# Kernel tuning notes

Hardware: AMD Instinct MI355X
Metric: run time of the kernel (lower is better)

Reference implementation:

```python
import jax, jax.numpy as jnp
import numpy as np

PS = 2      # patch_size
TOPK = 3    # topk


def setup_inputs() -> dict:
    key = jax.random.key(0)
    x = jax.random.normal(key, (16, 128, 64, 64), dtype=jnp.float32)
    alpha = jnp.asarray(5.0, dtype=jnp.float32)
    return {"x": x, "alpha": alpha}


def reference(x, alpha):
    ps = PS
    b, c, h, w = x.shape
    nph, npw = h // ps, w // ps
    npatch = nph * npw
    pa = ps * ps
    # F.normalize(x, p=2, dim=-3): L2-normalize over channels
    nrm = jnp.sqrt(jnp.sum(x * x, axis=1, keepdims=True))
    x = x / jnp.maximum(nrm, 1e-12)
    # patchify: [b,c,h,w] -> [b,c,num_patches,patch_area]
    x = x.reshape(b * c * nph, ps, npw, ps)
    x = jnp.swapaxes(x, 1, 2).reshape(b, c, npatch, pa)
    diag = np.arange(ps) * (ps + 1)          # diagonal positions within a patch
    x = x[:, :, :, diag]                     # [b,c,npatch,ps]
    x = jnp.swapaxes(x, 1, 3)                # [b,ps,npatch,c]
    # per-diagonal-pixel patch correlation matrix
    corr = jnp.einsum('bpnc,bpmc->bpnm', x, x)           # [b,ps,np,np]
    avg = jnp.mean(corr, axis=1, keepdims=True)
    corr = jnp.concatenate([corr, avg], axis=1)          # [b,ps+1,np,np]
    # gaussian self-suppression mask (1 - gaussian centered at each patch)
    rat_s = 0.05
    sr, sc = nph * rat_s, npw * rat_s
    ind_r = jnp.arange(nph, dtype=jnp.float32).reshape(1, nph, 1)
    ind_c = jnp.arange(npw, dtype=jnp.float32).reshape(1, 1, npw)
    cr, cc = jnp.meshgrid(jnp.arange(nph, dtype=jnp.float32),
                          jnp.arange(npw, dtype=jnp.float32), indexing='ij')
    cent_r = cr.reshape(npatch, 1, 1)
    cent_c = cc.reshape(npatch, 1, 1)
    g = jnp.exp(-(ind_r - cent_r) ** 2 / (2.0 * sr * sr)) \
        * jnp.exp(-(ind_c - cent_c) ** 2 / (2.0 * sc * sc))   # [np,nph,npw]
    mask = (1.0 - g).reshape(1, 1, npatch, npatch)
    s = (corr * mask) * alpha
    # dual (row + column) softmax
    a = jax.nn.softmax(s, axis=-1) * jax.nn.softmax(s, axis=-2)  # [b,ps+1,np,np]
    # scatter: diagonal in-patch pixels get their own map, rest get the avg map
    src = np.full(pa, ps, dtype=np.int64)
    src[diag] = np.arange(ps)
    a = a[:, src]                              # [b,pa,np,np]
    # un-patchify attention back to [b, npatch, h, w]
    a = jnp.swapaxes(a, 1, 3)                  # [b,np,np,pa]
    a = a.reshape(b * npatch * nph, npw, ps, ps)
    a = jnp.swapaxes(a, 1, 2)
    a = a.reshape(b, npatch, h, w)
    # top-k over the patch (correlation-source) dim
    vals = jax.lax.top_k(jnp.moveaxis(a, 1, -1), TOPK)[0]  # [b,h,w,k]
    return jnp.moveaxis(vals, -1, 1)           # [b,k,h,w]
```

## Files before the change

kernel.cpp:

```cpp
#include <hip/hip_runtime.h>
#include <math.h>

#define NB 16
#define NCH 128
#define NH 64
#define NW 64
#define NP 1024

#define TN 32
#define TM 128
#define KC 32
#define KP 36
#define PK 40

#define NTILE 144

typedef __attribute__((ext_vector_type(8))) short short8v;
typedef __attribute__((ext_vector_type(4))) float f32x4;

__device__ __forceinline__ float med3(float a, float b, float c) {
  return __builtin_amdgcn_fmed3f(a, b, c);
}
__device__ __forceinline__ void top3_ins(float& t0, float& t1, float& t2, float a) {
  float n0 = fmaxf(t0, a);
  float n1 = med3(a, t0, t1);
  float n2 = med3(a, t1, t2);
  t0 = n0; t1 = n1; t2 = n2;
}
__device__ __forceinline__ float dot4(float4 a, float4 b) {
  return a.x * b.x + a.y * b.y + a.z * b.z + a.w * b.w;
}
__device__ __forceinline__ ushort f2bf(float f) {
  unsigned u = __float_as_uint(f);
  unsigned r = (u + 0x7FFFu + ((u >> 16) & 1u)) >> 16;
  return (ushort)r;
}
__device__ __forceinline__ float bf2f(ushort h) {
  return __uint_as_float(((unsigned)h) << 16);
}

__global__ __launch_bounds__(256) void prep_split(const float* __restrict__ x,
                                                  ushort* __restrict__ Vs,
                                                  float* __restrict__ rsum) {
  int blk = blockIdx.x;
  int t = threadIdx.x;
  int gid = blk * 256 + t;
  if (gid < NB * 3 * NP) rsum[gid] = 0.f;

  int b = blk >> 5;
  int c = (blk >> 4) & 1;
  int ng = blk & 15;
  int nl = t >> 2;
  int kq = t & 3;
  int n = ng * 64 + nl;
  int i = 2 * (n >> 5) + c;
  int j = 2 * (n & 31) + c;
  const float* xp = x + (size_t)b * NCH * NH * NW + i * NW + j;

  float v[32];
#pragma unroll
  for (int e = 0; e < 32; ++e)
    v[e] = xp[(size_t)(kq * 32 + e) * NH * NW];

  float ss = 0.f;
#pragma unroll
  for (int e = 0; e < 32; ++e) ss += v[e] * v[e];
  ss += __shfl_xor(ss, 1, 64);
  ss += __shfl_xor(ss, 2, 64);
  float r = 1.0f / fmaxf(sqrtf(ss), 1e-12f);

  size_t base = ((size_t)(b * 2 + c) * 3) * NP * NCH + (size_t)n * NCH + kq * 32;
  ushort* p1 = Vs + base;
  ushort* p2 = Vs + base + (size_t)NP * NCH;
  ushort* p3 = Vs + base + (size_t)2 * NP * NCH;
#pragma unroll
  for (int kg2 = 0; kg2 < 4; ++kg2) {
    ushort h1[8], h2[8], h3[8];
#pragma unroll
    for (int e = 0; e < 8; ++e) {
      float vv = v[kg2 * 8 + e] * r;
      ushort a = f2bf(vv);
      float r1 = vv - bf2f(a);
      ushort bq = f2bf(r1);
      float r2 = r1 - bf2f(bq);
      ushort cq = f2bf(r2);
      h1[e] = a; h2[e] = bq; h3[e] = cq;
    }
    *(float4*)(p1 + kg2 * 8) = *(float4*)h1;
    *(float4*)(p2 + kg2 * 8) = *(float4*)h2;
    *(float4*)(p3 + kg2 * 8) = *(float4*)h3;
  }
}

__global__ __launch_bounds__(256, 2) void gemm_mfma(
    const ushort* __restrict__ Vs, const float* __restrict__ alpha_p,
    float2* __restrict__ Sbuf, float* __restrict__ rsum) {
  __shared__ __align__(16) char smem[2 * 3 * 32 * PK * 2 + 2 * 3 * 128 * PK * 2];
  ushort (*A_s)[3][32][PK] = reinterpret_cast<ushort(*)[3][32][PK]>(smem);
  ushort (*B_s)[3][128][PK] =
      reinterpret_cast<ushort(*)[3][128][PK]>(smem + 2 * 3 * 32 * PK * 2);
  float2 (*Ts)[33] = reinterpret_cast<float2(*)[33]>(smem);

  int wg = blockIdx.x;
  int xcd = wg & 7;
  int jj = wg >> 3;
  int half = (jj >= NTILE) ? 1 : 0;
  const int b = 2 * xcd + half;
  int id = jj - half * NTILE;
  int g = 0;
  while (id >= 4 * (8 - g)) { id -= 4 * (8 - g); ++g; }
  const int ni = 4 * g + id / (8 - g);
  const int mj = g + id % (8 - g);
  const int n0 = ni * TN;
  const int m0 = mj * TM;

  const int t = threadIdx.x;
  const int lane = t & 63, wv = t >> 6;
  const int jc = lane & 15, kg = lane >> 4;
  const float alpha = *alpha_p;
  const ushort* Vsb = Vs + (size_t)b * 6 * NP * NCH;
  float* rs = rsum + (size_t)b * 3 * NP;

  f32x4 acc[2][2][2];
#pragma unroll
  for (int c = 0; c < 2; ++c)
#pragma unroll
    for (int i = 0; i < 2; ++i)
#pragma unroll
      for (int j = 0; j < 2; ++j) acc[c][i][j] = (f32x4){0.f, 0.f, 0.f, 0.f};

  for (int k0 = 0; k0 < NCH; k0 += KC) {
    __syncthreads();
#pragma unroll
    for (int q = 0; q < 3; ++q) {
      int flat = q * 256 + t;
      int p = flat >> 7;
      int rem = flat & 127;
      int row = rem >> 2, u = rem & 3;
      const ushort* src = Vsb + ((size_t)p * NP + n0 + row) * NCH + k0 + u * 8;
      *(float4*)&A_s[p / 3][p % 3][row][u * 8] = *(const float4*)src;
    }
#pragma unroll
    for (int q = 0; q < 12; ++q) {
      int flat = q * 256 + t;
      int p = flat >> 9;
      int rem = flat & 511;
      int row = rem >> 2, u = rem & 3;
      const ushort* src = Vsb + ((size_t)p * NP + m0 + row) * NCH + k0 + u * 8;
      *(float4*)&B_s[p / 3][p % 3][row][u * 8] = *(const float4*)src;
    }
    __syncthreads();

#pragma unroll
    for (int c = 0; c < 2; ++c) {
      short8v a1n0 = *(const short8v*)&A_s[c][0][jc][kg * 8];
      short8v a1n1 = *(const short8v*)&A_s[c][0][16 + jc][kg * 8];
      short8v a2n0 = *(const short8v*)&A_s[c][1][jc][kg * 8];
      short8v a2n1 = *(const short8v*)&A_s[c][1][16 + jc][kg * 8];
      short8v a3n0 = *(const short8v*)&A_s[c][2][jc][kg * 8];
      short8v a3n1 = *(const short8v*)&A_s[c][2][16 + jc][kg * 8];
      {
        short8v b0 = *(const short8v*)&B_s[c][0][wv * 32 + jc][kg * 8];
        short8v b1 = *(const short8v*)&B_s[c][0][wv * 32 + 16 + jc][kg * 8];
        acc[c][0][0] = __builtin_amdgcn_mfma_f32_16x16x32_bf16(a1n0, b0, acc[c][0][0], 0, 0, 0);
        acc[c][1][0] = __builtin_amdgcn_mfma_f32_16x16x32_bf16(a1n1, b0, acc[c][1][0], 0, 0, 0);
        acc[c][0][1] = __builtin_amdgcn_mfma_f32_16x16x32_bf16(a1n0, b1, acc[c][0][1], 0, 0, 0);
        acc[c][1][1] = __builtin_amdgcn_mfma_f32_16x16x32_bf16(a1n1, b1, acc[c][1][1], 0, 0, 0);
        acc[c][0][0] = __builtin_amdgcn_mfma_f32_16x16x32_bf16(a2n0, b0, acc[c][0][0], 0, 0, 0);
        acc[c][1][0] = __builtin_amdgcn_mfma_f32_16x16x32_bf16(a2n1, b0, acc[c][1][0], 0, 0, 0);
        acc[c][0][1] = __builtin_amdgcn_mfma_f32_16x16x32_bf16(a2n0, b1, acc[c][0][1], 0, 0, 0);
        acc[c][1][1] = __builtin_amdgcn_mfma_f32_16x16x32_bf16(a2n1, b1, acc[c][1][1], 0, 0, 0);
        acc[c][0][0] = __builtin_amdgcn_mfma_f32_16x16x32_bf16(a3n0, b0, acc[c][0][0], 0, 0, 0);
        acc[c][1][0] = __builtin_amdgcn_mfma_f32_16x16x32_bf16(a3n1, b0, acc[c][1][0], 0, 0, 0);
        acc[c][0][1] = __builtin_amdgcn_mfma_f32_16x16x32_bf16(a3n0, b1, acc[c][0][1], 0, 0, 0);
        acc[c][1][1] = __builtin_amdgcn_mfma_f32_16x16x32_bf16(a3n1, b1, acc[c][1][1], 0, 0, 0);
      }
      {
        short8v b0 = *(const short8v*)&B_s[c][1][wv * 32 + jc][kg * 8];
        short8v b1 = *(const short8v*)&B_s[c][1][wv * 32 + 16 + jc][kg * 8];
        acc[c][0][0] = __builtin_amdgcn_mfma_f32_16x16x32_bf16(a1n0, b0, acc[c][0][0], 0, 0, 0);
        acc[c][1][0] = __builtin_amdgcn_mfma_f32_16x16x32_bf16(a1n1, b0, acc[c][1][0], 0, 0, 0);
        acc[c][0][1] = __builtin_amdgcn_mfma_f32_16x16x32_bf16(a1n0, b1, acc[c][0][1], 0, 0, 0);
        acc[c][1][1] = __builtin_amdgcn_mfma_f32_16x16x32_bf16(a1n1, b1, acc[c][1][1], 0, 0, 0);
        acc[c][0][0] = __builtin_amdgcn_mfma_f32_16x16x32_bf16(a2n0, b0, acc[c][0][0], 0, 0, 0);
        acc[c][1][0] = __builtin_amdgcn_mfma_f32_16x16x32_bf16(a2n1, b0, acc[c][1][0], 0, 0, 0);
        acc[c][0][1] = __builtin_amdgcn_mfma_f32_16x16x32_bf16(a2n0, b1, acc[c][0][1], 0, 0, 0);
        acc[c][1][1] = __builtin_amdgcn_mfma_f32_16x16x32_bf16(a2n1, b1, acc[c][1][1], 0, 0, 0);
      }
      {
        short8v b0 = *(const short8v*)&B_s[c][2][wv * 32 + jc][kg * 8];
        short8v b1 = *(const short8v*)&B_s[c][2][wv * 32 + 16 + jc][kg * 8];
        acc[c][0][0] = __builtin_amdgcn_mfma_f32_16x16x32_bf16(a1n0, b0, acc[c][0][0], 0, 0, 0);
        acc[c][1][0] = __builtin_amdgcn_mfma_f32_16x16x32_bf16(a1n1, b0, acc[c][1][0], 0, 0, 0);
        acc[c][0][1] = __builtin_amdgcn_mfma_f32_16x16x32_bf16(a1n0, b1, acc[c][0][1], 0, 0, 0);
        acc[c][1][1] = __builtin_amdgcn_mfma_f32_16x16x32_bf16(a1n1, b1, acc[c][1][1], 0, 0, 0);
      }
    }
  }

  __syncthreads();
  float e[2][4][3];
#pragma unroll
  for (int ns = 0; ns < 2; ++ns)
#pragma unroll
    for (int r = 0; r < 4; ++r)
#pragma unroll
      for (int c = 0; c < 3; ++c) e[ns][r][c] = 0.f;

#pragma unroll
  for (int ns = 0; ns < 2; ++ns) {
#pragma unroll
    for (int r = 0; r < 4; ++r) {
      int nl = ns * 16 + kg * 4 + r;
      int n = n0 + nl;
      int nr = n >> 5, nc = n & 31;
      float2* rowp = Sbuf + ((size_t)b * NP + n) * NP;
#pragma unroll
      for (int ms = 0; ms < 2; ++ms) {
        int ml = wv * 32 + ms * 16 + jc;
        int m = m0 + ml;
        int dr = nr - (m >> 5);
        int dc = nc - (m & 31);
        float gss = __expf(-(float)(dr * dr + dc * dc) * 0.1953125f);
        float wgt = (1.0f - gss) * alpha;
        float2 sv = make_float2(acc[0][ns][ms][r] * wgt, acc[1][ns][ms][r] * wgt);
        Ts[ml][nl] = sv;
        if (m >= n) {
          rowp[m] = sv;
          e[ns][r][0] += __expf(sv.x);
          e[ns][r][1] += __expf(sv.y);
          e[ns][r][2] += __expf(0.5f * (sv.x + sv.y));
        }
      }
    }
  }
#pragma unroll
  for (int off = 1; off < 16; off <<= 1) {
#pragma unroll
    for (int ns = 0; ns < 2; ++ns)
#pragma unroll
      for (int r = 0; r < 4; ++r)
#pragma unroll
        for (int c = 0; c < 3; ++c)
          e[ns][r][c] += __shfl_xor(e[ns][r][c], off, 64);
  }
  if (jc == 0) {
#pragma unroll
    for (int ns = 0; ns < 2; ++ns)
#pragma unroll
      for (int r = 0; r < 4; ++r)
#pragma unroll
        for (int c = 0; c < 3; ++c)
          atomicAdd(&rs[(size_t)c * NP + (n0 + ns * 16 + kg * 4 + r)], e[ns][r][c]);
  }

  __syncthreads();
#pragma unroll
  for (int q = 0; q < 16; ++q) {
    int flat = q * 256 + t;
    int ml = flat >> 5;
    int r = flat & 31;
    int m = m0 + ml;
    int n = n0 + r;
    if (m > n) Sbuf[((size_t)b * NP + m) * NP + n] = Ts[ml][r];
  }
  {
    int ml = t >> 1;
    int rh = (t & 1) * 16;
    int m = m0 + ml;
    float e0 = 0.f, e1 = 0.f, e2 = 0.f;
#pragma unroll
    for (int rr = 0; rr < 16; ++rr) {
      int r = rh + rr;
      int n = n0 + r;
      float2 sv = Ts[ml][r];
      if (m > n) {
        e0 += __expf(sv.x);
        e1 += __expf(sv.y);
        e2 += __expf(0.5f * (sv.x + sv.y));
      }
    }
    e0 += __shfl_xor(e0, 1, 64);
    e1 += __shfl_xor(e1, 1, 64);
    e2 += __shfl_xor(e2, 1, 64);
    if ((t & 1) == 0) {
      atomicAdd(&rs[(size_t)0 * NP + m], e0);
      atomicAdd(&rs[(size_t)1 * NP + m], e1);
      atomicAdd(&rs[(size_t)2 * NP + m], e2);
    }
  }
}

__global__ __launch_bounds__(256) void recip_kernel(float* __restrict__ p, int nelem) {
  int i = blockIdx.x * 256 + threadIdx.x;
  if (i < nelem) p[i] = 1.0f / p[i];
}

__global__ __launch_bounds__(256, 4) void topk_kernel(
    const float2* __restrict__ Sbuf, const float* __restrict__ rinv,
    float* __restrict__ out) {
  const int n = blockIdx.x, b = blockIdx.y;
  const int t = threadIdx.x;
  const float* rb = rinv + (size_t)b * 3 * NP;
  float rin[3];
#pragma unroll
  for (int c = 0; c < 3; ++c) rin[c] = rb[c * NP + n];
  const float2* row = Sbuf + ((size_t)b * NP + n) * NP;

  float t0[3] = {0.f, 0.f, 0.f}, t1[3] = {0.f, 0.f, 0.f}, t2[3] = {0.f, 0.f, 0.f};
#pragma unroll
  for (int q = 0; q < 4; ++q) {
    int m = t + q * 256;
    float2 s01 = row[m];
    float s[3];
    s[0] = s01.x; s[1] = s01.y; s[2] = 0.5f * (s01.x + s01.y);
#pragma unroll
    for (int c = 0; c < 3; ++c) {
      float a = __expf(2.0f * s[c]) * rin[c] * rb[c * NP + m];
      top3_ins(t0[c], t1[c], t2[c], a);
    }
  }
#pragma unroll
  for (int off = 1; off < 64; off <<= 1) {
#pragma unroll
    for (int c = 0; c < 3; ++c) {
      float o0 = __shfl_xor(t0[c], off, 64);
      float o1 = __shfl_xor(t1[c], off, 64);
      float o2 = __shfl_xor(t2[c], off, 64);
      top3_ins(t0[c], t1[c], t2[c], o0);
      top3_ins(t0[c], t1[c], t2[c], o1);
      top3_ins(t0[c], t1[c], t2[c], o2);
    }
  }
  __shared__ float lds[4][9];
  if ((t & 63) == 0) {
    int w = t >> 6;
#pragma unroll
    for (int c = 0; c < 3; ++c) {
      lds[w][c * 3 + 0] = t0[c];
      lds[w][c * 3 + 1] = t1[c];
      lds[w][c * 3 + 2] = t2[c];
    }
  }
  __syncthreads();
  if (t == 0) {
#pragma unroll
    for (int w = 1; w < 4; ++w)
#pragma unroll
      for (int c = 0; c < 3; ++c) {
        top3_ins(t0[c], t1[c], t2[c], lds[w][c * 3 + 0]);
        top3_ins(t0[c], t1[c], t2[c], lds[w][c * 3 + 1]);
        top3_ins(t0[c], t1[c], t2[c], lds[w][c * 3 + 2]);
      }
    int pr = n >> 5, pc = n & 31;
#pragma unroll
    for (int c = 0; c < 3; ++c) {
      int ii0, jj0, ii1 = -1, jj1 = -1;
      if (c == 0)      { ii0 = 2 * pr;     jj0 = 2 * pc; }
      else if (c == 1) { ii0 = 2 * pr + 1; jj0 = 2 * pc + 1; }
      else             { ii0 = 2 * pr;     jj0 = 2 * pc + 1;
                         ii1 = 2 * pr + 1; jj1 = 2 * pc; }
      out[(((size_t)b * 3 + 0) * NH + ii0) * NW + jj0] = t0[c];
      out[(((size_t)b * 3 + 1) * NH + ii0) * NW + jj0] = t1[c];
      out[(((size_t)b * 3 + 2) * NH + ii0) * NW + jj0] = t2[c];
      if (ii1 >= 0) {
        out[(((size_t)b * 3 + 0) * NH + ii1) * NW + jj1] = t0[c];
        out[(((size_t)b * 3 + 1) * NH + ii1) * NW + jj1] = t1[c];
        out[(((size_t)b * 3 + 2) * NH + ii1) * NW + jj1] = t2[c];
      }
    }
  }
}

__global__ __launch_bounds__(256) void prep_kernel(const float* __restrict__ x,
                                                   float* __restrict__ V) {
  int blk = blockIdx.x;
  int t = threadIdx.x;
  int b = blk >> 3;
  int c = (blk >> 2) & 1;
  int n = (blk & 3) * 256 + t;
  int i = 2 * (n >> 5) + c;
  int j = 2 * (n & 31) + c;
  const float* xp = x + (size_t)b * NCH * NH * NW + i * NW + j;
  float ss = 0.f;
#pragma unroll 8
  for (int ch = 0; ch < NCH; ++ch) {
    float v = xp[(size_t)ch * NH * NW];
    ss += v * v;
  }
  float r = 1.0f / fmaxf(sqrtf(ss), 1e-12f);
  float* vp = V + (((size_t)b * 2 + c) * NP + n) * NCH;
#pragma unroll 8
  for (int ch = 0; ch < NCH; ++ch) {
    vp[ch] = xp[(size_t)ch * NH * NW] * r;
  }
}

template <int PASS>
__global__ __launch_bounds__(256, 2) void corr_kernel(
    const float* __restrict__ V, const float* __restrict__ alpha_p,
    float* __restrict__ rsum_g, float* __restrict__ out) {
  __shared__ __align__(16) float As[2][TN][KP];
  __shared__ __align__(16) float Bs[2][TM][KP];

  const int b = blockIdx.y;
  const int n0 = blockIdx.x * TN;
  const int t = threadIdx.x;
  const int tx = t & 31;
  const int ty = t >> 5;
  const float alpha = *alpha_p;
  const float* Vb = V + (size_t)b * 2 * NP * NCH;

  float sm[3][4];
  float t0[3][4], t1[3][4], t2[3][4];
  float rin[3][4];
#pragma unroll
  for (int c = 0; c < 3; ++c)
#pragma unroll
    for (int i = 0; i < 4; ++i) {
      sm[c][i] = 0.f;
      t0[c][i] = 0.f; t1[c][i] = 0.f; t2[c][i] = 0.f;
    }
  if (PASS == 2) {
#pragma unroll
    for (int c = 0; c < 3; ++c)
#pragma unroll
      for (int i = 0; i < 4; ++i) {
        int n = n0 + ty * 4 + i;
        rin[c][i] = 1.0f / rsum_g[((size_t)b * 3 + c) * NP + n];
      }
  }

  for (int mc = 0; mc < NP / TM; ++mc) {
    const int m0 = mc * TM;
    float acc[2][4][4];
#pragma unroll
    for (int c = 0; c < 2; ++c)
#pragma unroll
      for (int i = 0; i < 4; ++i)
#pragma unroll
        for (int j = 0; j < 4; ++j) acc[c][i][j] = 0.f;

    for (int k0 = 0; k0 < NCH; k0 += KC) {
      __syncthreads();
#pragma unroll
      for (int q = 0; q < 2; ++q) {
        int flat = q * 256 + t;
        int c = flat >> 8;
        int rem = flat & 255;
        int row = rem >> 3;
        int kgx = rem & 7;
        float4 v4 = *(const float4*)(Vb + ((size_t)c * NP + n0 + row) * NCH + k0 + kgx * 4);
        *(float4*)&As[c][row][kgx * 4] = v4;
      }
#pragma unroll
      for (int q = 0; q < 8; ++q) {
        int flat = q * 256 + t;
        int c = flat >> 10;
        int rem = flat & 1023;
        int row = rem >> 3;
        int kgx = rem & 7;
        float4 v4 = *(const float4*)(Vb + ((size_t)c * NP + m0 + row) * NCH + k0 + kgx * 4);
        *(float4*)&Bs[c][row][kgx * 4] = v4;
      }
      __syncthreads();

      for (int kgx = 0; kgx < KC; kgx += 4) {
        float4 a4[2][4], b4[2][4];
#pragma unroll
        for (int c = 0; c < 2; ++c)
#pragma unroll
          for (int i = 0; i < 4; ++i)
            a4[c][i] = *(const float4*)&As[c][ty * 4 + i][kgx];
#pragma unroll
        for (int c = 0; c < 2; ++c)
#pragma unroll
          for (int j = 0; j < 4; ++j)
            b4[c][j] = *(const float4*)&Bs[c][tx + 32 * j][kgx];
#pragma unroll
        for (int c = 0; c < 2; ++c)
#pragma unroll
          for (int i = 0; i < 4; ++i)
#pragma unroll
            for (int j = 0; j < 4; ++j)
              acc[c][i][j] += dot4(a4[c][i], b4[c][j]);
      }
    }

    float rim[3][4];
    if (PASS == 2) {
#pragma unroll
      for (int c = 0; c < 3; ++c)
#pragma unroll
        for (int j = 0; j < 4; ++j) {
          int m = m0 + tx + 32 * j;
          rim[c][j] = 1.0f / rsum_g[((size_t)b * 3 + c) * NP + m];
        }
    }
#pragma unroll
    for (int i = 0; i < 4; ++i) {
      int n = n0 + ty * 4 + i;
      int nr = n >> 5, nc = n & 31;
      float s[3][4];
#pragma unroll
      for (int j = 0; j < 4; ++j) {
        int m = m0 + tx + 32 * j;
        int dr = nr - (m >> 5);
        int dc = nc - (m & 31);
        float gq = __expf(-(float)(dr * dr + dc * dc) * 0.1953125f);
        float wgt = (1.0f - gq) * alpha;
        float s0v = acc[0][i][j] * wgt;
        float s1v = acc[1][i][j] * wgt;
        s[0][j] = s0v; s[1][j] = s1v; s[2][j] = 0.5f * (s0v + s1v);
      }
      if (PASS == 1) {
#pragma unroll
        for (int c = 0; c < 3; ++c) {
          sm[c][i] += __expf(s[c][0]) + __expf(s[c][1]) +
                      __expf(s[c][2]) + __expf(s[c][3]);
        }
      } else {
#pragma unroll
        for (int c = 0; c < 3; ++c) {
#pragma unroll
          for (int j = 0; j < 4; ++j) {
            float a = __expf(2.0f * s[c][j]) * rin[c][i] * rim[c][j];
            top3_ins(t0[c][i], t1[c][i], t2[c][i], a);
          }
        }
      }
    }
  }

  if (PASS == 1) {
#pragma unroll
    for (int off = 1; off < 32; off <<= 1) {
#pragma unroll
      for (int c = 0; c < 3; ++c)
#pragma unroll
        for (int i = 0; i < 4; ++i)
          sm[c][i] += __shfl_xor(sm[c][i], off, 64);
    }
    if (tx == 0) {
#pragma unroll
      for (int c = 0; c < 3; ++c)
#pragma unroll
        for (int i = 0; i < 4; ++i) {
          int n = n0 + ty * 4 + i;
          rsum_g[((size_t)b * 3 + c) * NP + n] = sm[c][i];
        }
    }
  } else {
#pragma unroll
    for (int off = 1; off < 32; off <<= 1) {
#pragma unroll
      for (int c = 0; c < 3; ++c)
#pragma unroll
        for (int i = 0; i < 4; ++i) {
          float o0 = __shfl_xor(t0[c][i], off, 64);
          float o1 = __shfl_xor(t1[c][i], off, 64);
          float o2 = __shfl_xor(t2[c][i], off, 64);
          top3_ins(t0[c][i], t1[c][i], t2[c][i], o0);
          top3_ins(t0[c][i], t1[c][i], t2[c][i], o1);
          top3_ins(t0[c][i], t1[c][i], t2[c][i], o2);
        }
    }
    if (tx == 0) {
#pragma unroll
      for (int c = 0; c < 3; ++c)
#pragma unroll
        for (int i = 0; i < 4; ++i) {
          int n = n0 + ty * 4 + i;
          int pr = n >> 5, pc = n & 31;
          float v0 = t0[c][i], v1 = t1[c][i], v2 = t2[c][i];
          int ii0, jj0, ii1 = -1, jj1 = -1;
          if (c == 0)      { ii0 = 2 * pr;     jj0 = 2 * pc; }
          else if (c == 1) { ii0 = 2 * pr + 1; jj0 = 2 * pc + 1; }
          else             { ii0 = 2 * pr;     jj0 = 2 * pc + 1;
                             ii1 = 2 * pr + 1; jj1 = 2 * pc; }
          out[(((size_t)b * 3 + 0) * NH + ii0) * NW + jj0] = v0;
          out[(((size_t)b * 3 + 1) * NH + ii0) * NW + jj0] = v1;
          out[(((size_t)b * 3 + 2) * NH + ii0) * NW + jj0] = v2;
          if (ii1 >= 0) {
            out[(((size_t)b * 3 + 0) * NH + ii1) * NW + jj1] = v0;
            out[(((size_t)b * 3 + 1) * NH + ii1) * NW + jj1] = v1;
            out[(((size_t)b * 3 + 2) * NH + ii1) * NW + jj1] = v2;
          }
        }
    }
  }
}

extern "C" void kernel_launch(void* const* d_in, const int* in_sizes, int n_in,
                              void* d_out, int out_size, void* d_ws, size_t ws_size,
                              hipStream_t stream) {
  const float* x = (const float*)d_in[0];
  const float* alpha = (const float*)d_in[1];
  float* out = (float*)d_out;

  const size_t nVsU = (size_t)NB * 6 * NP * NCH;
  const size_t nRs = (size_t)NB * 3 * NP;
  const size_t nS = (size_t)NB * NP * NP;

  ushort* Vs = (ushort*)d_ws;
  float* rsum = (float*)(Vs + nVsU);
  float2* Sbuf = (float2*)(rsum + nRs);

  const size_t need_bytes = nVsU * 2 + nRs * 4 + nS * 8;

  if (ws_size >= need_bytes) {
    prep_split<<<512, 256, 0, stream>>>(x, Vs, rsum);
    gemm_mfma<<<NTILE * NB, 256, 0, stream>>>(Vs, alpha, Sbuf, rsum);
    recip_kernel<<<(NB * 3 * NP + 255) / 256, 256, 0, stream>>>(rsum, NB * 3 * NP);
    topk_kernel<<<dim3(NP, NB), 256, 0, stream>>>(Sbuf, rsum, out);
  } else {
    float* V = (float*)d_ws;
    float* rsum_f = V + (size_t)NB * 2 * NP * NCH;
    prep_kernel<<<128, 256, 0, stream>>>(x, V);
    corr_kernel<1><<<dim3(NP / TN, NB), 256, 0, stream>>>(V, alpha, rsum_f, out);
    corr_kernel<2><<<dim3(NP / TN, NB), 256, 0, stream>>>(V, alpha, rsum_f, out);
  }
}
```

Baseline: 154.7 us.

## Process the two diagonal channels sequentially to halve LDS and raise occupancy

The GEMM loop now iterates over the two diagonal-pixel maps one after another, staging only one map's A/B tiles in shared memory at a time. This halves the LDS footprint, and launch bounds are raised from 2 to 4 blocks per CU to use the extra occupancy. The cost is twice as many K-loop iterations, each with its own barrier pair, and smaller loads per stage. The 4-block bound may also force the compiler to use fewer registers and spill.

```diff
diff --git a/kernel.cpp b/kernel.cpp
--- a/kernel.cpp
+++ b/kernel.cpp
@@ -92,13 +92,13 @@
   }
 }
 
-__global__ __launch_bounds__(256, 2) void gemm_mfma(
+__global__ __launch_bounds__(256, 4) void gemm_mfma(
     const ushort* __restrict__ Vs, const float* __restrict__ alpha_p,
     float2* __restrict__ Sbuf, float* __restrict__ rsum) {
-  __shared__ __align__(16) char smem[2 * 3 * 32 * PK * 2 + 2 * 3 * 128 * PK * 2];
-  ushort (*A_s)[3][32][PK] = reinterpret_cast<ushort(*)[3][32][PK]>(smem);
-  ushort (*B_s)[3][128][PK] =
-      reinterpret_cast<ushort(*)[3][128][PK]>(smem + 2 * 3 * 32 * PK * 2);
+  __shared__ __align__(16) char smem[3 * 32 * PK * 2 + 3 * 128 * PK * 2];
+  ushort (*A_s)[32][PK] = reinterpret_cast<ushort(*)[32][PK]>(smem);
+  ushort (*B_s)[128][PK] =
+      reinterpret_cast<ushort(*)[128][PK]>(smem + 3 * 32 * PK * 2);
   float2 (*Ts)[33] = reinterpret_cast<float2(*)[33]>(smem);
 
   int wg = blockIdx.x;
@@ -129,39 +129,41 @@
 #pragma unroll
       for (int j = 0; j < 2; ++j) acc[c][i][j] = (f32x4){0.f, 0.f, 0.f, 0.f};
 
-  for (int k0 = 0; k0 < NCH; k0 += KC) {
-    __syncthreads();
-#pragma unroll
-    for (int q = 0; q < 3; ++q) {
-      int flat = q * 256 + t;
-      int p = flat >> 7;
-      int rem = flat & 127;
-      int row = rem >> 2, u = rem & 3;
-      const ushort* src = Vsb + ((size_t)p * NP + n0 + row) * NCH + k0 + u * 8;
-      *(float4*)&A_s[p / 3][p % 3][row][u * 8] = *(const float4*)src;
-    }
-#pragma unroll
-    for (int q = 0; q < 12; ++q) {
-      int flat = q * 256 + t;
-      int p = flat >> 9;
-      int rem = flat & 511;
-      int row = rem >> 2, u = rem & 3;
-      const ushort* src = Vsb + ((size_t)p * NP + m0 + row) * NCH + k0 + u * 8;
-      *(float4*)&B_s[p / 3][p % 3][row][u * 8] = *(const float4*)src;
-    }
-    __syncthreads();
-
-#pragma unroll
-    for (int c = 0; c < 2; ++c) {
-      short8v a1n0 = *(const short8v*)&A_s[c][0][jc][kg * 8];
-      short8v a1n1 = *(const short8v*)&A_s[c][0][16 + jc][kg * 8];
-      short8v a2n0 = *(const short8v*)&A_s[c][1][jc][kg * 8];
-      short8v a2n1 = *(const short8v*)&A_s[c][1][16 + jc][kg * 8];
-      short8v a3n0 = *(const short8v*)&A_s[c][2][jc][kg * 8];
-      short8v a3n1 = *(const short8v*)&A_s[c][2][16 + jc][kg * 8];
+#pragma unroll
+  for (int c = 0; c < 2; ++c) {
+    for (int k0 = 0; k0 < NCH; k0 += KC) {
+      __syncthreads();
+#pragma unroll
+      for (int q = 0; q < 2; ++q) {
+        int flat = q * 256 + t;
+        if (flat < 384) {
+          int p = flat >> 7;
+          int rem = flat & 127;
+          int row = rem >> 2, u = rem & 3;
+          const ushort* src = Vsb + ((size_t)(c * 3 + p) * NP + n0 + row) * NCH + k0 + u * 8;
+          *(float4*)&A_s[p][row][u * 8] = *(const float4*)src;
+        }
+      }
+#pragma unroll
+      for (int q = 0; q < 6; ++q) {
+        int flat = q * 256 + t;
+        int p = flat >> 9;
+        int rem = flat & 511;
+        int row = rem >> 2, u = rem & 3;
+        const ushort* src = Vsb + ((size_t)(c * 3 + p) * NP + m0 + row) * NCH + k0 + u * 8;
+        *(float4*)&B_s[p][row][u * 8] = *(const float4*)src;
+      }
+      __syncthreads();
+
+      short8v a1n0 = *(const short8v*)&A_s[0][jc][kg * 8];
+      short8v a1n1 = *(const short8v*)&A_s[0][16 + jc][kg * 8];
+      short8v a2n0 = *(const short8v*)&A_s[1][jc][kg * 8];
+      short8v a2n1 = *(const short8v*)&A_s[1][16 + jc][kg * 8];
+      short8v a3n0 = *(const short8v*)&A_s[2][jc][kg * 8];
+      short8v a3n1 = *(const short8v*)&A_s[2][16 + jc][kg * 8];
       {
-        short8v b0 = *(const short8v*)&B_s[c][0][wv * 32 + jc][kg * 8];
-        short8v b1 = *(const short8v*)&B_s[c][0][wv * 32 + 16 + jc][kg * 8];
+        short8v b0 = *(const short8v*)&B_s[0][wv * 32 + jc][kg * 8];
+        short8v b1 = *(const short8v*)&B_s[0][wv * 32 + 16 + jc][kg * 8];
         acc[c][0][0] = __builtin_amdgcn_mfma_f32_16x16x32_bf16(a1n0, b0, acc[c][0][0], 0, 0, 0);
         acc[c][1][0] = __builtin_amdgcn_mfma_f32_16x16x32_bf16(a1n1, b0, acc[c][1][0], 0, 0, 0);
         acc[c][0][1] = __builtin_amdgcn_mfma_f32_16x16x32_bf16(a1n0, b1, acc[c][0][1], 0, 0, 0);
@@ -176,8 +178,8 @@
         acc[c][1][1] = __builtin_amdgcn_mfma_f32_16x16x32_bf16(a3n1, b1, acc[c][1][1], 0, 0, 0);
       }
       {
-        short8v b0 = *(const short8v*)&B_s[c][1][wv * 32 + jc][kg * 8];
-        short8v b1 = *(const short8v*)&B_s[c][1][wv * 32 + 16 + jc][kg * 8];
+        short8v b0 = *(const short8v*)&B_s[1][wv * 32 + jc][kg * 8];
+        short8v b1 = *(const short8v*)&B_s[1][wv * 32 + 16 + jc][kg * 8];
         acc[c][0][0] = __builtin_amdgcn_mfma_f32_16x16x32_bf16(a1n0, b0, acc[c][0][0], 0, 0, 0);
         acc[c][1][0] = __builtin_amdgcn_mfma_f32_16x16x32_bf16(a1n1, b0, acc[c][1][0], 0, 0, 0);
         acc[c][0][1] = __builtin_amdgcn_mfma_f32_16x16x32_bf16(a1n0, b1, acc[c][0][1], 0, 0, 0);
@@ -188,8 +190,8 @@
         acc[c][1][1] = __builtin_amdgcn_mfma_f32_16x16x32_bf16(a2n1, b1, acc[c][1][1], 0, 0, 0);
       }
       {
-        short8v b0 = *(const short8v*)&B_s[c][2][wv * 32 + jc][kg * 8];
-        short8v b1 = *(const short8v*)&B_s[c][2][wv * 32 + 16 + jc][kg * 8];
+        short8v b0 = *(const short8v*)&B_s[2][wv * 32 + jc][kg * 8];
+        short8v b1 = *(const short8v*)&B_s[2][wv * 32 + 16 + jc][kg * 8];
         acc[c][0][0] = __builtin_amdgcn_mfma_f32_16x16x32_bf16(a1n0, b0, acc[c][0][0], 0, 0, 0);
         acc[c][1][0] = __builtin_amdgcn_mfma_f32_16x16x32_bf16(a1n1, b0, acc[c][1][0], 0, 0, 0);
         acc[c][0][1] = __builtin_amdgcn_mfma_f32_16x16x32_bf16(a1n0, b1, acc[c][0][1], 0, 0, 0);
```

New measurement: 148.4 us. 4.1% less time.
